# Optimization experiments

Measured on AMD Instinct MI355X. Metric: run time of the kernel, lower is better.

Reference implementation:

```python
import jax, jax.numpy as jnp
import numpy as np
from jax import lax

TH = 1.0      # float threshold from __init__
TAU = 0.1     # forward default
EPS_BN = 1e-5
EPS_NORM = 1e-8


def setup_inputs() -> dict:
    key = jax.random.key(0)
    ks = jax.random.split(key, 9)
    B, C, T, N = 1, 256, 128, 256
    HID = 32
    return {
        'v_rel': jax.random.normal(ks[0], (B, C, T, N), jnp.float32),
        'w1': jax.random.normal(ks[1], (HID, 2), jnp.float32) * 0.05,
        'b1': jax.random.normal(ks[2], (HID,), jnp.float32) * 0.05,
        'bn_gamma': jax.random.uniform(ks[3], (HID,), jnp.float32) + 0.5,
        'bn_beta': jax.random.normal(ks[4], (HID,), jnp.float32) * 0.05,
        'bn_mean': jax.random.normal(ks[5], (HID,), jnp.float32) * 0.05,
        'bn_var': jax.random.uniform(ks[6], (HID,), jnp.float32) + 0.5,
        'w2': jax.random.normal(ks[7], (1, HID), jnp.float32) * 0.05,
        'b2': jax.random.normal(ks[8], (1,), jnp.float32) * 0.05,
    }


def _per_ch(p):
    return p[None, :, None, None]


def _dist_mat(v_rel, w1, b1, bn_gamma, bn_beta, bn_mean, bn_var, w2, b2):
    # d_type == 'learned': pairwise diffs of last-frame absolute features (first 2 channels)
    x = v_rel[:, :2, -1, :]                       # (1, 2, N)
    d = x[:, :, :, None] - x[:, :, None, :]       # (1, 2, N, N) == reshaped temp
    h = jnp.einsum('oi,binm->bonm', w1, d) + _per_ch(b1)   # 1x1 conv -> (1, HID, N, N)
    h = jax.nn.relu(h)
    # BatchNorm2d, inference mode with running stats
    h = (h - _per_ch(bn_mean)) * (_per_ch(bn_gamma) / jnp.sqrt(_per_ch(bn_var) + EPS_BN)) + _per_ch(bn_beta)
    h = jnp.exp(jnp.einsum('oi,binm->bonm', w2, h) + _per_ch(b2))  # (1, 1, N, N)
    dm = 0.5 * (h + jnp.swapaxes(h, -1, -2))      # mean of stack(temp, temp^T)
    return dm[:, 0].mean(axis=0)                  # squeeze(1).mean(dim=0) -> (N, N)


def _find_group_indices(dist, th):
    # Serial union-find over strictly-lower-triangular close pairs in row-major
    # order, exactly matching the torch loop semantics; expressed as lax.scan.
    N = dist.shape[0]
    flat = jnp.arange(N * N)
    r = flat // N
    c = flat % N
    ok = (c < r) & (dist[r, c] <= th)

    def step(labels, inp):
        ri, ci, o = inp
        merged = jnp.where(labels == labels[ri], labels[ci], labels)
        return jnp.where(o, merged, labels), None

    labels, _ = lax.scan(step, jnp.arange(N), (r, c, ok))
    # relabel sorted-unique labels to 0..K-1 (labels are in [0, N))
    present = jnp.zeros(N, jnp.int32).at[labels].set(1)
    ranks = jnp.cumsum(present) - 1
    return ranks[labels]


def reference(v_rel, w1, b1, bn_gamma, bn_beta, bn_mean, bn_var, w2, b2):
    B, C, T, N = v_rel.shape
    dm = _dist_mat(v_rel, w1, b1, bn_gamma, bn_beta, bn_mean, bn_var, w2, b2)  # (N, N)
    group_indices = _find_group_indices(dm, TH)[None]                          # (1, N)
    # group_backprop_trick with tau=0.1, hard=True (straight-through)
    sig = jax.nn.sigmoid(-(dm - TH) / TAU)
    sig_norm = sig / (sig.sum(axis=0, keepdims=True) + EPS_NORM)
    v = v_rel[0]                                                               # (C, T, N)
    v_soft = jnp.einsum('ctn,nm->ctm', v, sig_norm)
    v_grouped = (lax.stop_gradient(v - v_soft) + v_soft)[None]                 # (1, C, T, N)
    dist_mat_full = jnp.broadcast_to(dm[None, None], (B, T, N, N))
    return v_grouped, group_indices, dist_mat_full
```

## Files before the change

### kernel.cpp

```cpp
#include <hip/hip_runtime.h>
#include <stdint.h>

#define NN 256
#define TT 128
#define CC 256
#define TH_F 1.0f
#define EPS_BN_F 1e-5f

#define OUT0_ELEMS (CC * TT * NN)
#define OUT1_OFF   OUT0_ELEMS
#define OUT2_OFF   (OUT0_ELEMS + NN)

#define N0_F4      (OUT0_ELEMS / 4)
#define CHUNK_F4   1024
#define COPY0_BLKS (N0_F4 / CHUNK_F4)

typedef float vfloat4 __attribute__((ext_vector_type(4)));

__global__ __launch_bounds__(256) void k1_bulk(
        const float* __restrict__ v_rel,
        const float* __restrict__ w1,
        const float* __restrict__ b1,
        const float* __restrict__ bn_g,
        const float* __restrict__ bn_b,
        const float* __restrict__ bn_m,
        const float* __restrict__ bn_v,
        const float* __restrict__ w2,
        const float* __restrict__ b2,
        float* __restrict__ out) {
    const int tid = threadIdx.x;
    const int bid = blockIdx.x;

    if (bid < NN) {
        __shared__ float row[256];
        const int m = tid;
        const int n = bid;
        const float x0n = v_rel[127 * 256 + n];
        const float x0m = v_rel[127 * 256 + m];
        const float x1n = v_rel[255 * 256 + n];
        const float x1m = v_rel[255 * 256 + m];
        const float d0 = x0n - x0m;
        const float d1 = x1n - x1m;
        float accF = 0.0f, accB = 0.0f;
        #pragma unroll
        for (int o = 0; o < 32; ++o) {
            const float w10 = w1[2 * o], w11 = w1[2 * o + 1];
            const float scale = bn_g[o] / sqrtf(bn_v[o] + EPS_BN_F);
            const float mu = bn_m[o], be = bn_b[o], bb = b1[o], a = w2[o];
            float preF = w10 * d0 + w11 * d1 + bb;
            float preB = w10 * (-d0) + w11 * (-d1) + bb;
            float hF = fmaxf(preF, 0.0f);
            float hB = fmaxf(preB, 0.0f);
            accF += a * ((hF - mu) * scale + be);
            accB += a * ((hB - mu) * scale + be);
        }
        const float sF = expf(accF + b2[0]);
        const float sB = expf(accB + b2[0]);
        const float val = 0.5f * (sF + sB);

        float* __restrict__ o2 = out + OUT2_OFF;
        o2[n * 256 + m] = val;
        row[m] = val;
        __syncthreads();
        const vfloat4 v4 = *reinterpret_cast<const vfloat4*>(&row[(tid & 63) * 4]);
        const int f4i = tid & 63;
        for (int t = 1 + (tid >> 6); t < TT; t += 4) {
            vfloat4* dst = reinterpret_cast<vfloat4*>(o2 + t * (NN * NN) + n * 256);
            __builtin_nontemporal_store(v4, dst + f4i);
        }
    } else {
        const int base = (bid - NN) * CHUNK_F4 + tid;
        const vfloat4* __restrict__ in4 = reinterpret_cast<const vfloat4*>(v_rel);
        vfloat4* __restrict__ o0 = reinterpret_cast<vfloat4*>(out);
        #pragma unroll
        for (int q = 0; q < 4; ++q) {
            const int i = base + q * 256;
            __builtin_nontemporal_store(in4[i], o0 + i);
        }
    }
}

__device__ __forceinline__ uint32_t rl32(uint32_t v, uint32_t l) {
    return (uint32_t)__builtin_amdgcn_readlane((int)v, (int)l);
}
__device__ __forceinline__ uint64_t rl64(uint64_t v, uint32_t l) {
    uint32_t lo = rl32((uint32_t)v, l);
    uint32_t hi = rl32((uint32_t)(v >> 32), l);
    return ((uint64_t)hi << 32) | lo;
}

template<int NW>
__device__ __forceinline__ uint32_t pick_lab(uint32_t lab0, uint32_t lab1,
                                             uint32_t lab2, uint32_t lab3,
                                             uint32_t p) {
    const uint32_t ls = p & 63u;
    uint32_t a = rl32(lab0, ls);
    if (NW == 1) return a;
    uint32_t b = rl32(lab1, ls);
    const uint32_t g = (p >> 6) & 3u;
    if (NW == 2) return (g & 1u) ? b : a;
    uint32_t c = rl32(lab2, ls);
    uint32_t d = (NW > 3) ? rl32(lab3, ls) : c;
    uint32_t ab = (g & 1u) ? b : a;
    uint32_t cd = (g & 1u) ? d : c;
    return (g & 2u) ? cd : ab;
}

template<int NW>
__device__ __forceinline__ void scan_chunk(const int K, const int lane,
                                           uint32_t& lab0, uint32_t& lab1,
                                           uint32_t& lab2, uint32_t& lab3,
                                           uint32_t& labw,
                                           const uint64_t* __restrict__ bits,
                                           bool& fast, uint32_t& V) {
    const int base = (K * 64 + lane) * 4;
    uint64_t Wr0 = bits[base + 0];
    uint64_t Wr1 = (NW > 1) ? bits[base + 1] : 0;
    uint64_t Wr2 = (NW > 2) ? bits[base + 2] : 0;
    uint64_t Wr3 = (NW > 3) ? bits[base + 3] : 0;

    const uint64_t rowOr = Wr0 | Wr1 | Wr2 | Wr3;
    const uint64_t nonempty = __ballot(rowOr != 0);

    if (fast && nonempty == ~0ull) {
        labw = V;
        return;
    }

    for (int rr = 0; rr < 64; ++rr) {
        const bool rowEmpty = ((nonempty >> rr) & 1ull) == 0ull;
        if (fast) {
            if (!rowEmpty) {
                labw = ((uint32_t)lane == (uint32_t)rr) ? V : labw;
                continue;
            }
            fast = (V == (uint32_t)(K * 64 + rr));
            continue;
        }
        const uint64_t w0 = rl64(Wr0, (uint32_t)rr);
        const uint64_t w1 = (NW > 1) ? rl64(Wr1, (uint32_t)rr) : 0;
        const uint64_t w2 = (NW > 2) ? rl64(Wr2, (uint32_t)rr) : 0;
        const uint64_t w3 = (NW > 3) ? rl64(Wr3, (uint32_t)rr) : 0;
        uint32_t f0 = w0 ? (uint32_t)__builtin_ctzll(w0) : 512u;
        uint32_t p = f0;
        if (NW > 1) { uint32_t f = w1 ? (uint32_t)__builtin_ctzll(w1) + 64u  : 512u; p = p < f ? p : f; }
        if (NW > 2) { uint32_t f = w2 ? (uint32_t)__builtin_ctzll(w2) + 128u : 512u; p = p < f ? p : f; }
        if (NW > 3) { uint32_t f = w3 ? (uint32_t)__builtin_ctzll(w3) + 192u : 512u; p = p < f ? p : f; }
        const uint32_t lc = pick_lab<NW>(lab0, lab1, lab2, lab3, p & 255u);
        const uint32_t upd = (p < 256u) ? (uint32_t)rr : 64u;
        labw = ((uint32_t)lane == upd) ? lc : labw;
        uint32_t cur = lc;
        uint64_t R0, R1 = 0, R2 = 0, R3 = 0;
        for (;;) {
            R0 = __ballot(lab0 != cur);
            if (NW > 1) R1 = __ballot(lab1 != cur);
            if (NW > 2) R2 = __ballot(lab2 != cur);
            if (NW > 3) R3 = __ballot(lab3 != cur);
            const uint64_t Q0 = R0 & w0;
            const uint64_t Q1 = (NW > 1) ? (R1 & w1) : 0;
            const uint64_t Q2 = (NW > 2) ? (R2 & w2) : 0;
            const uint64_t Q3 = (NW > 3) ? (R3 & w3) : 0;
            if (!(Q0 | Q1 | Q2 | Q3)) break;
            uint32_t h0 = Q0 ? (uint32_t)__builtin_ctzll(Q0) : 512u;
            uint32_t p2 = h0;
            if (NW > 1) { uint32_t h = Q1 ? (uint32_t)__builtin_ctzll(Q1) + 64u  : 512u; p2 = p2 < h ? p2 : h; }
            if (NW > 2) { uint32_t h = Q2 ? (uint32_t)__builtin_ctzll(Q2) + 128u : 512u; p2 = p2 < h ? p2 : h; }
            if (NW > 3) { uint32_t h = Q3 ? (uint32_t)__builtin_ctzll(Q3) + 192u : 512u; p2 = p2 < h ? p2 : h; }
            const uint32_t lc2 = pick_lab<NW>(lab0, lab1, lab2, lab3, p2);
            lab0 = (lab0 == cur) ? lc2 : lab0;
            if (NW > 1) lab1 = (lab1 == cur) ? lc2 : lab1;
            if (NW > 2) lab2 = (lab2 == cur) ? lc2 : lab2;
            if (NW > 3) lab3 = (lab3 == cur) ? lc2 : lab3;
            cur = lc2;
        }
        const uint64_t pmK = (rr == 63) ? ~0ull : ((1ull << (rr + 1)) - 1ull);
        uint64_t nb = R0 & ((NW - 1 == 0) ? pmK : ~0ull);
        if (NW > 1) nb |= R1 & ((NW - 1 == 1) ? pmK : ~0ull);
        if (NW > 2) nb |= R2 & ((NW - 1 == 2) ? pmK : ~0ull);
        if (NW > 3) nb |= R3 & pmK;
        if (nb == 0) { fast = true; V = cur; }
    }
}

__global__ __launch_bounds__(256) void k2_scan(float* __restrict__ out) {
    const int tid = threadIdx.x;
    const float* __restrict__ dm = out + OUT2_OFF;

    __shared__ __align__(16) uint64_t bits[1024];
    __shared__ uint32_t lab_arr[256];
    __shared__ uint32_t pres[256];
    __shared__ uint32_t rnk[256];

    for (int i = 0; i < 4; ++i) {
        const int wid = i * 256 + tid;
        const int r = wid >> 2;
        const int gw = wid & 3;
        uint64_t bm = 0;
        const int cbase = gw * 64;
        if (cbase < r) {
            const float4* p = reinterpret_cast<const float4*>(dm + r * 256 + cbase);
            #pragma unroll
            for (int q = 0; q < 16; ++q) {
                const float4 v = p[q];
                const int c0 = cbase + q * 4;
                if (c0 + 0 < r && v.x <= TH_F) bm |= 1ull << (q * 4 + 0);
                if (c0 + 1 < r && v.y <= TH_F) bm |= 1ull << (q * 4 + 1);
                if (c0 + 2 < r && v.z <= TH_F) bm |= 1ull << (q * 4 + 2);
                if (c0 + 3 < r && v.w <= TH_F) bm |= 1ull << (q * 4 + 3);
            }
        }
        bits[wid] = bm;
    }
    __syncthreads();

    if (tid < 64) {
        const int lane = tid;
        uint32_t lab0 = (uint32_t)lane;
        uint32_t lab1 = (uint32_t)(64 + lane);
        uint32_t lab2 = (uint32_t)(128 + lane);
        uint32_t lab3 = (uint32_t)(192 + lane);
        bool fast = true;
        uint32_t V = 0;

        scan_chunk<1>(0, lane, lab0, lab1, lab2, lab3, lab0, bits, fast, V);
        scan_chunk<2>(1, lane, lab0, lab1, lab2, lab3, lab1, bits, fast, V);
        scan_chunk<3>(2, lane, lab0, lab1, lab2, lab3, lab2, bits, fast, V);
        scan_chunk<4>(3, lane, lab0, lab1, lab2, lab3, lab3, bits, fast, V);

        lab_arr[lane]       = lab0;
        lab_arr[64 + lane]  = lab1;
        lab_arr[128 + lane] = lab2;
        lab_arr[192 + lane] = lab3;
    }
    __syncthreads();

    pres[tid] = 0;
    __syncthreads();
    pres[lab_arr[tid]] = 1;
    __syncthreads();
    if (tid < 64) {
        const int lane = tid;
        const int c0 = 4 * lane;
        const uint32_t t0 = pres[c0 + 0];
        const uint32_t t1 = pres[c0 + 1];
        const uint32_t t2 = pres[c0 + 2];
        const uint32_t t3 = pres[c0 + 3];
        const uint32_t s0 = t0, s1 = s0 + t1, s2 = s1 + t2, s3 = s2 + t3;
        uint32_t incl = s3;
        #pragma unroll
        for (int off = 1; off < 64; off <<= 1) {
            uint32_t u = __shfl_up(incl, off);
            if (lane >= off) incl += u;
        }
        const uint32_t excl = incl - s3;
        rnk[c0 + 0] = excl + s0 - 1;
        rnk[c0 + 1] = excl + s1 - 1;
        rnk[c0 + 2] = excl + s2 - 1;
        rnk[c0 + 3] = excl + s3 - 1;
    }
    __syncthreads();
    out[OUT1_OFF + tid] = (float)rnk[lab_arr[tid]];
}

extern "C" void kernel_launch(void* const* d_in, const int* in_sizes, int n_in,
                              void* d_out, int out_size, void* d_ws, size_t ws_size,
                              hipStream_t stream) {
    const float* v_rel = (const float*)d_in[0];
    const float* w1    = (const float*)d_in[1];
    const float* b1    = (const float*)d_in[2];
    const float* bn_g  = (const float*)d_in[3];
    const float* bn_b  = (const float*)d_in[4];
    const float* bn_m  = (const float*)d_in[5];
    const float* bn_v  = (const float*)d_in[6];
    const float* w2    = (const float*)d_in[7];
    const float* b2    = (const float*)d_in[8];
    float* out = (float*)d_out;

    k1_bulk<<<NN + COPY0_BLKS, 256, 0, stream>>>(v_rel, w1, b1, bn_g, bn_b,
                                                 bn_m, bn_v, w2, b2, out);
    k2_scan<<<1, 256, 0, stream>>>(out);
}
```

Before: 117.7 us.

## Fuse distance and union-find kernels with atomic counter handoff

Merges the distance/broadcast kernel and the single-block union-find scan into one launch. A dedicated scan block spins on a global atomic counter until all 256 distance rows are published, so the serial scan overlaps with the bulk broadcast and copy stores. This adds a memset or init launch for the counter and relies on the scan block not starving producer blocks. Every block now also carries the larger shared-memory footprint.

```diff
diff --git a/kernel.cpp b/kernel.cpp
--- a/kernel.cpp
+++ b/kernel.cpp
@@ -14,70 +14,13 @@
 #define N0_F4      (OUT0_ELEMS / 4)
 #define CHUNK_F4   1024
 #define COPY0_BLKS (N0_F4 / CHUNK_F4)
+#define SCAN_BID   NN
+#define GRID_BLKS  (NN + 1 + COPY0_BLKS)
 
 typedef float vfloat4 __attribute__((ext_vector_type(4)));
 
-__global__ __launch_bounds__(256) void k1_bulk(
-        const float* __restrict__ v_rel,
-        const float* __restrict__ w1,
-        const float* __restrict__ b1,
-        const float* __restrict__ bn_g,
-        const float* __restrict__ bn_b,
-        const float* __restrict__ bn_m,
-        const float* __restrict__ bn_v,
-        const float* __restrict__ w2,
-        const float* __restrict__ b2,
-        float* __restrict__ out) {
-    const int tid = threadIdx.x;
-    const int bid = blockIdx.x;
-
-    if (bid < NN) {
-        __shared__ float row[256];
-        const int m = tid;
-        const int n = bid;
-        const float x0n = v_rel[127 * 256 + n];
-        const float x0m = v_rel[127 * 256 + m];
-        const float x1n = v_rel[255 * 256 + n];
-        const float x1m = v_rel[255 * 256 + m];
-        const float d0 = x0n - x0m;
-        const float d1 = x1n - x1m;
-        float accF = 0.0f, accB = 0.0f;
-        #pragma unroll
-        for (int o = 0; o < 32; ++o) {
-            const float w10 = w1[2 * o], w11 = w1[2 * o + 1];
-            const float scale = bn_g[o] / sqrtf(bn_v[o] + EPS_BN_F);
-            const float mu = bn_m[o], be = bn_b[o], bb = b1[o], a = w2[o];
-            float preF = w10 * d0 + w11 * d1 + bb;
-            float preB = w10 * (-d0) + w11 * (-d1) + bb;
-            float hF = fmaxf(preF, 0.0f);
-            float hB = fmaxf(preB, 0.0f);
-            accF += a * ((hF - mu) * scale + be);
-            accB += a * ((hB - mu) * scale + be);
-        }
-        const float sF = expf(accF + b2[0]);
-        const float sB = expf(accB + b2[0]);
-        const float val = 0.5f * (sF + sB);
-
-        float* __restrict__ o2 = out + OUT2_OFF;
-        o2[n * 256 + m] = val;
-        row[m] = val;
-        __syncthreads();
-        const vfloat4 v4 = *reinterpret_cast<const vfloat4*>(&row[(tid & 63) * 4]);
-        const int f4i = tid & 63;
-        for (int t = 1 + (tid >> 6); t < TT; t += 4) {
-            vfloat4* dst = reinterpret_cast<vfloat4*>(o2 + t * (NN * NN) + n * 256);
-            __builtin_nontemporal_store(v4, dst + f4i);
-        }
-    } else {
-        const int base = (bid - NN) * CHUNK_F4 + tid;
-        const vfloat4* __restrict__ in4 = reinterpret_cast<const vfloat4*>(v_rel);
-        vfloat4* __restrict__ o0 = reinterpret_cast<vfloat4*>(out);
-        #pragma unroll
-        for (int q = 0; q < 4; ++q) {
-            const int i = base + q * 256;
-            __builtin_nontemporal_store(in4[i], o0 + i);
-        }
-    }
+__global__ void init_cnt(float* __restrict__ out) {
+    if (threadIdx.x == 0) *(uint32_t*)(out + OUT1_OFF) = 0u;
 }
 
 __device__ __forceinline__ uint32_t rl32(uint32_t v, uint32_t l) {
@@ -182,84 +125,157 @@
     }
 }
 
-__global__ __launch_bounds__(256) void k2_scan(float* __restrict__ out) {
+__global__ __launch_bounds__(256) void fused(
+        const float* __restrict__ v_rel,
+        const float* __restrict__ w1,
+        const float* __restrict__ b1,
+        const float* __restrict__ bn_g,
+        const float* __restrict__ bn_b,
+        const float* __restrict__ bn_m,
+        const float* __restrict__ bn_v,
+        const float* __restrict__ w2,
+        const float* __restrict__ b2,
+        float* __restrict__ out,
+        uint32_t* __restrict__ cnt) {
     const int tid = threadIdx.x;
-    const float* __restrict__ dm = out + OUT2_OFF;
+    const int bid = blockIdx.x;
+    float* __restrict__ o2 = out + OUT2_OFF;
 
     __shared__ __align__(16) uint64_t bits[1024];
     __shared__ uint32_t lab_arr[256];
     __shared__ uint32_t pres[256];
     __shared__ uint32_t rnk[256];
-
-    for (int i = 0; i < 4; ++i) {
-        const int wid = i * 256 + tid;
-        const int r = wid >> 2;
-        const int gw = wid & 3;
-        uint64_t bm = 0;
-        const int cbase = gw * 64;
-        if (cbase < r) {
-            const float4* p = reinterpret_cast<const float4*>(dm + r * 256 + cbase);
+    __shared__ float row[256];
+
+    if (bid < NN) {
+        const int m = tid;
+        const int n = bid;
+        const float x0n = v_rel[127 * 256 + n];
+        const float x0m = v_rel[127 * 256 + m];
+        const float x1n = v_rel[255 * 256 + n];
+        const float x1m = v_rel[255 * 256 + m];
+        const float d0 = x0n - x0m;
+        const float d1 = x1n - x1m;
+        float accF = 0.0f, accB = 0.0f;
+        #pragma unroll
+        for (int o = 0; o < 32; ++o) {
+            const float w10 = w1[2 * o], w11 = w1[2 * o + 1];
+            const float scale = bn_g[o] / sqrtf(bn_v[o] + EPS_BN_F);
+            const float mu = bn_m[o], be = bn_b[o], bb = b1[o], a = w2[o];
+            float preF = w10 * d0 + w11 * d1 + bb;
+            float preB = w10 * (-d0) + w11 * (-d1) + bb;
+            float hF = fmaxf(preF, 0.0f);
+            float hB = fmaxf(preB, 0.0f);
+            accF += a * ((hF - mu) * scale + be);
+            accB += a * ((hB - mu) * scale + be);
+        }
+        const float sF = expf(accF + b2[0]);
+        const float sB = expf(accB + b2[0]);
+        const float val = 0.5f * (sF + sB);
+
+        row[m] = val;
+        o2[n * 256 + m] = val;
+        __threadfence();
+        __syncthreads();
+        if (tid == 0) atomicAdd(cnt, 1u);
+
+        const vfloat4 v4 = *reinterpret_cast<const vfloat4*>(&row[(tid & 63) * 4]);
+        const int f4i = tid & 63;
+        for (int t = 1 + (tid >> 6); t < TT; t += 4) {
+            vfloat4* dst = reinterpret_cast<vfloat4*>(o2 + t * (NN * NN) + n * 256);
+            __builtin_nontemporal_store(v4, dst + f4i);
+        }
+    } else if (bid == SCAN_BID) {
+        if (tid == 0) {
+            while (__hip_atomic_load(cnt, __ATOMIC_RELAXED,
+                                     __HIP_MEMORY_SCOPE_AGENT) < (uint32_t)NN)
+                __builtin_amdgcn_s_sleep(8);
+            (void)__hip_atomic_load(cnt, __ATOMIC_ACQUIRE,
+                                    __HIP_MEMORY_SCOPE_AGENT);
+        }
+        __syncthreads();
+        __threadfence();
+
+        const float* __restrict__ dm = o2;
+        for (int i = 0; i < 4; ++i) {
+            const int wid = i * 256 + tid;
+            const int r = wid >> 2;
+            const int gw = wid & 3;
+            uint64_t bm = 0;
+            const int cbase = gw * 64;
+            if (cbase < r) {
+                const float4* p = reinterpret_cast<const float4*>(dm + r * 256 + cbase);
+                #pragma unroll
+                for (int q = 0; q < 16; ++q) {
+                    const float4 v = p[q];
+                    const int c0 = cbase + q * 4;
+                    if (c0 + 0 < r && v.x <= TH_F) bm |= 1ull << (q * 4 + 0);
+                    if (c0 + 1 < r && v.y <= TH_F) bm |= 1ull << (q * 4 + 1);
+                    if (c0 + 2 < r && v.z <= TH_F) bm |= 1ull << (q * 4 + 2);
+                    if (c0 + 3 < r && v.w <= TH_F) bm |= 1ull << (q * 4 + 3);
+                }
+            }
+            bits[wid] = bm;
+        }
+        __syncthreads();
+
+        if (tid < 64) {
+            const int lane = tid;
+            uint32_t lab0 = (uint32_t)lane;
+            uint32_t lab1 = (uint32_t)(64 + lane);
+            uint32_t lab2 = (uint32_t)(128 + lane);
+            uint32_t lab3 = (uint32_t)(192 + lane);
+            bool fast = true;
+            uint32_t V = 0;
+
+            scan_chunk<1>(0, lane, lab0, lab1, lab2, lab3, lab0, bits, fast, V);
+            scan_chunk<2>(1, lane, lab0, lab1, lab2, lab3, lab1, bits, fast, V);
+            scan_chunk<3>(2, lane, lab0, lab1, lab2, lab3, lab2, bits, fast, V);
+            scan_chunk<4>(3, lane, lab0, lab1, lab2, lab3, lab3, bits, fast, V);
+
+            lab_arr[lane]       = lab0;
+            lab_arr[64 + lane]  = lab1;
+            lab_arr[128 + lane] = lab2;
+            lab_arr[192 + lane] = lab3;
+        }
+        __syncthreads();
+
+        pres[tid] = 0;
+        __syncthreads();
+        pres[lab_arr[tid]] = 1;
+        __syncthreads();
+        if (tid < 64) {
+            const int lane = tid;
+            const int c0 = 4 * lane;
+            const uint32_t t0 = pres[c0 + 0];
+            const uint32_t t1 = pres[c0 + 1];
+            const uint32_t t2 = pres[c0 + 2];
+            const uint32_t t3 = pres[c0 + 3];
+            const uint32_t s0 = t0, s1 = s0 + t1, s2 = s1 + t2, s3 = s2 + t3;
+            uint32_t incl = s3;
             #pragma unroll
-            for (int q = 0; q < 16; ++q) {
-                const float4 v = p[q];
-                const int c0 = cbase + q * 4;
-                if (c0 + 0 < r && v.x <= TH_F) bm |= 1ull << (q * 4 + 0);
-                if (c0 + 1 < r && v.y <= TH_F) bm |= 1ull << (q * 4 + 1);
-                if (c0 + 2 < r && v.z <= TH_F) bm |= 1ull << (q * 4 + 2);
-                if (c0 + 3 < r && v.w <= TH_F) bm |= 1ull << (q * 4 + 3);
+            for (int off = 1; off < 64; off <<= 1) {
+                uint32_t u = __shfl_up(incl, off);
+                if (lane >= off) incl += u;
             }
-        }
-        bits[wid] = bm;
+            const uint32_t excl = incl - s3;
+            rnk[c0 + 0] = excl + s0 - 1;
+            rnk[c0 + 1] = excl + s1 - 1;
+            rnk[c0 + 2] = excl + s2 - 1;
+            rnk[c0 + 3] = excl + s3 - 1;
+        }
+        __syncthreads();
+        out[OUT1_OFF + tid] = (float)rnk[lab_arr[tid]];
+    } else {
+        const int base = (bid - NN - 1) * CHUNK_F4 + tid;
+        const vfloat4* __restrict__ in4 = reinterpret_cast<const vfloat4*>(v_rel);
+        vfloat4* __restrict__ o0 = reinterpret_cast<vfloat4*>(out);
+        #pragma unroll
+        for (int q = 0; q < 4; ++q) {
+            const int i = base + q * 256;
+            __builtin_nontemporal_store(in4[i], o0 + i);
+        }
     }
-    __syncthreads();
-
-    if (tid < 64) {
-        const int lane = tid;
-        uint32_t lab0 = (uint32_t)lane;
-        uint32_t lab1 = (uint32_t)(64 + lane);
-        uint32_t lab2 = (uint32_t)(128 + lane);
-        uint32_t lab3 = (uint32_t)(192 + lane);
-        bool fast = true;
-        uint32_t V = 0;
-
-        scan_chunk<1>(0, lane, lab0, lab1, lab2, lab3, lab0, bits, fast, V);
-        scan_chunk<2>(1, lane, lab0, lab1, lab2, lab3, lab1, bits, fast, V);
-        scan_chunk<3>(2, lane, lab0, lab1, lab2, lab3, lab2, bits, fast, V);
-        scan_chunk<4>(3, lane, lab0, lab1, lab2, lab3, lab3, bits, fast, V);
-
-        lab_arr[lane]       = lab0;
-        lab_arr[64 + lane]  = lab1;
-        lab_arr[128 + lane] = lab2;
-        lab_arr[192 + lane] = lab3;
-    }
-    __syncthreads();
-
-    pres[tid] = 0;
-    __syncthreads();
-    pres[lab_arr[tid]] = 1;
-    __syncthreads();
-    if (tid < 64) {
-        const int lane = tid;
-        const int c0 = 4 * lane;
-        const uint32_t t0 = pres[c0 + 0];
-        const uint32_t t1 = pres[c0 + 1];
-        const uint32_t t2 = pres[c0 + 2];
-        const uint32_t t3 = pres[c0 + 3];
-        const uint32_t s0 = t0, s1 = s0 + t1, s2 = s1 + t2, s3 = s2 + t3;
-        uint32_t incl = s3;
-        #pragma unroll
-        for (int off = 1; off < 64; off <<= 1) {
-            uint32_t u = __shfl_up(incl, off);
-            if (lane >= off) incl += u;
-        }
-        const uint32_t excl = incl - s3;
-        rnk[c0 + 0] = excl + s0 - 1;
-        rnk[c0 + 1] = excl + s1 - 1;
-        rnk[c0 + 2] = excl + s2 - 1;
-        rnk[c0 + 3] = excl + s3 - 1;
-    }
-    __syncthreads();
-    out[OUT1_OFF + tid] = (float)rnk[lab_arr[tid]];
 }
 
 extern "C" void kernel_launch(void* const* d_in, const int* in_sizes, int n_in,
@@ -276,7 +292,14 @@
     const float* b2    = (const float*)d_in[8];
     float* out = (float*)d_out;
 
-    k1_bulk<<<NN + COPY0_BLKS, 256, 0, stream>>>(v_rel, w1, b1, bn_g, bn_b,
-                                                 bn_m, bn_v, w2, b2, out);
-    k2_scan<<<1, 256, 0, stream>>>(out);
-}
+    uint32_t* cnt;
+    if (d_ws != nullptr && ws_size >= 4) {
+        cnt = (uint32_t*)d_ws;
+        hipMemsetAsync(d_ws, 0, 4, stream);
+    } else {
+        cnt = (uint32_t*)(out + OUT1_OFF);
+        init_cnt<<<1, 64, 0, stream>>>(out);
+    }
+    fused<<<GRID_BLKS, 256, 0, stream>>>(v_rel, w1, b1, bn_g, bn_b, bn_m,
+                                         bn_v, w2, b2, out, cnt);
+}
```

Result: slower. 136.8 us (+16.2%).
